# Kernel optimization log

Measured on AMD Instinct MI355X. Metric: run time of the kernel, lower is better.

## Reference

```python
import jax, jax.numpy as jnp
import numpy as np

EPS = 1e-6


def _mlp(x, W1, b1, W2, b2):
    # x: [b,s]; W1: [m,s,h]; W2: [m,h,o] -> [m,b,o]  (m = stacked module dim)
    h = jnp.tanh(jnp.einsum('bs,msh->mbh', x, W1) + b1[:, None, :])
    return jnp.einsum('mbh,mho->mbo', h, W2) + b2[:, None, :]


def _ln(x, g, b):
    mu = jnp.mean(x, axis=-1, keepdims=True)
    var = jnp.var(x, axis=-1, keepdims=True)
    return g * (x - mu) / jnp.sqrt(var + EPS) + b


def setup_inputs() -> dict:
    B, S, H, E, R, L = 1024, 256, 512, 64, 32, 9
    key = jax.random.key(0)
    ks = jax.random.split(key, 8)

    def xavier(k, shape):
        bound = np.sqrt(6.0 / (shape[-2] + shape[-1])).astype(np.float32)
        return jax.random.uniform(k, shape, jnp.float32, -bound, bound)

    return {
        'query_embed': jax.random.normal(ks[0], (B, S), jnp.float32),
        'tpr': jax.random.normal(ks[1], (B, E, R, E), jnp.float32) * 0.1,
        'eW1': xavier(ks[2], (2, S, H)), 'eb1': jnp.zeros((2, H), jnp.float32),
        'eW2': xavier(ks[3], (2, H, E)), 'eb2': jnp.zeros((2, E), jnp.float32),
        'rW1': xavier(ks[4], (3, S, H)), 'rb1': jnp.zeros((3, H), jnp.float32),
        'rW2': xavier(ks[5], (3, H, R)), 'rb2': jnp.zeros((3, R), jnp.float32),
        'ln_g': jnp.ones((3, E), jnp.float32), 'ln_b': jnp.zeros((3, E), jnp.float32),
        'Z': xavier(ks[6], (E, L)),
    }


def reference(query_embed, tpr, eW1, eb1, eW2, eb2, rW1, rb1, rW2, rb2, ln_g, ln_b, Z):
    e = _mlp(query_embed, eW1, eb1, eW2, eb2)   # [2,B,E] (e[1] unused, as in original)
    r = _mlp(query_embed, rW1, rb1, rW2, rb2)   # [3,B,R]
    i1 = _ln(jnp.einsum('be,br,berf->bf', e[0], r[0], tpr), ln_g[0], ln_b[0])
    i2 = _ln(jnp.einsum('be,br,berf->bf', i1, r[1], tpr), ln_g[1], ln_b[1])
    i3 = _ln(jnp.einsum('be,br,berf->bf', i2, r[2], tpr), ln_g[2], ln_b[2])
    step_sum = i1 + i2 + i3
    return jnp.einsum('bf,fl->bl', step_sum, Z)
```

## Files before the change

### kernel.cpp

```cpp
#include <hip/hip_runtime.h>
#include <math.h>

#define B_  1024
#define S_  256
#define H_  512
#define E_  64
#define R_  32
#define L_  9
#define EPS_ 1e-6f
#define TB  16

__global__ __launch_bounds__(256) void mlp_kernel(
    const float* __restrict__ x,
    const float* __restrict__ eW1, const float* __restrict__ eb1,
    const float* __restrict__ eW2, const float* __restrict__ eb2,
    const float* __restrict__ rW1, const float* __restrict__ rb1,
    const float* __restrict__ rW2, const float* __restrict__ rb2,
    float* __restrict__ e0_out,
    float* __restrict__ r_out)
{
    __shared__ float xs[TB][S_];
    __shared__ float hs[TB][H_];
    const int t  = threadIdx.x;
    const int b0 = blockIdx.x * TB;
    const int m  = blockIdx.y;

    #pragma unroll
    for (int i = 0; i < TB; ++i)
        xs[i][t] = x[(size_t)(b0 + i) * S_ + t];
    __syncthreads();

    const float* W1 = (m == 0) ? eW1 : (rW1 + (size_t)(m - 1) * S_ * H_);
    const float* b1 = (m == 0) ? eb1 : (rb1 + (size_t)(m - 1) * H_);

    float acc0[TB], acc1[TB];
    #pragma unroll
    for (int bb = 0; bb < TB; ++bb) { acc0[bb] = 0.0f; acc1[bb] = 0.0f; }

    for (int s = 0; s < S_; ++s) {
        float w0 = W1[(size_t)s * H_ + t];
        float w1 = W1[(size_t)s * H_ + t + 256];
        #pragma unroll
        for (int bb = 0; bb < TB; ++bb) {
            float xv = xs[bb][s];
            acc0[bb] = fmaf(xv, w0, acc0[bb]);
            acc1[bb] = fmaf(xv, w1, acc1[bb]);
        }
    }
    float bias0 = b1[t], bias1 = b1[t + 256];
    #pragma unroll
    for (int bb = 0; bb < TB; ++bb) {
        hs[bb][t]       = tanhf(acc0[bb] + bias0);
        hs[bb][t + 256] = tanhf(acc1[bb] + bias1);
    }
    __syncthreads();

    if (m == 0) {
        const float* W2 = eW2;
        const float* b2 = eb2;
        int o  = t & 63;
        int bq = t >> 6;
        #pragma unroll
        for (int i = 0; i < TB / 4; ++i) {
            int bb = bq + i * 4;
            float acc = b2[o];
            for (int j = 0; j < H_; ++j)
                acc = fmaf(hs[bb][j], W2[(size_t)j * E_ + o], acc);
            e0_out[(size_t)(b0 + bb) * E_ + o] = acc;
        }
    } else {
        const float* W2 = rW2 + (size_t)(m - 1) * H_ * R_;
        const float* b2 = rb2 + (size_t)(m - 1) * R_;
        int o  = t & 31;
        int bq = t >> 5;
        #pragma unroll
        for (int i = 0; i < TB / 8; ++i) {
            int bb = bq + i * 8;
            float acc = b2[o];
            for (int j = 0; j < H_; ++j)
                acc = fmaf(hs[bb][j], W2[(size_t)j * R_ + o], acc);
            r_out[((size_t)(m - 1) * B_ + (b0 + bb)) * R_ + o] = acc;
        }
    }
}

__global__ __launch_bounds__(256) void tpr_kernel(
    const float* __restrict__ tpr,
    const float* __restrict__ e0,
    const float* __restrict__ rws,
    const float* __restrict__ ln_g,
    const float* __restrict__ ln_b,
    const float* __restrict__ Z,
    float* __restrict__ out)
{
    __shared__ __align__(16) float M[3][E_][E_];
    __shared__ float xcur[E_];
    __shared__ float ssum_sh[E_];
    __shared__ float rsh[3][R_];

    const int t = threadIdx.x;
    const int b = blockIdx.x;

    if (t < 96) { int k = t >> 5, j = t & 31; rsh[k][j] = rws[((size_t)k * B_ + b) * R_ + j]; }
    if (t < E_) xcur[t] = e0[(size_t)b * E_ + t];
    __syncthreads();

    const float4* tpr4 = (const float4*)(tpr + (size_t)b * E_ * R_ * E_);
    const int f4 = t & 15;
    const int eg = t >> 4;

    #pragma unroll
    for (int ep = 0; ep < 4; ++ep) {
        int e = eg + 16 * ep;
        float4 a0 = {0, 0, 0, 0}, a1 = {0, 0, 0, 0}, a2 = {0, 0, 0, 0};
        for (int r = 0; r < R_; ++r) {
            float4 v = tpr4[e * 512 + r * 16 + f4];
            float w0 = rsh[0][r], w1 = rsh[1][r], w2 = rsh[2][r];
            a0.x = fmaf(w0, v.x, a0.x); a0.y = fmaf(w0, v.y, a0.y);
            a0.z = fmaf(w0, v.z, a0.z); a0.w = fmaf(w0, v.w, a0.w);
            a1.x = fmaf(w1, v.x, a1.x); a1.y = fmaf(w1, v.y, a1.y);
            a1.z = fmaf(w1, v.z, a1.z); a1.w = fmaf(w1, v.w, a1.w);
            a2.x = fmaf(w2, v.x, a2.x); a2.y = fmaf(w2, v.y, a2.y);
            a2.z = fmaf(w2, v.z, a2.z); a2.w = fmaf(w2, v.w, a2.w);
        }
        ((float4*)&M[0][e][0])[f4] = a0;
        ((float4*)&M[1][e][0])[f4] = a1;
        ((float4*)&M[2][e][0])[f4] = a2;
    }
    __syncthreads();

    float ssum = 0.0f;
    for (int k = 0; k < 3; ++k) {
        float iv = 0.0f;
        if (t < E_) {
            const int f = t;
            float acc = 0.0f;
            for (int e = 0; e < E_; ++e)
                acc = fmaf(xcur[e], M[k][e][f], acc);
            float s = acc;
            #pragma unroll
            for (int off = 32; off >= 1; off >>= 1) s += __shfl_xor(s, off, 64);
            float mu = s * (1.0f / 64.0f);
            float d = acc - mu;
            float vs = d * d;
            #pragma unroll
            for (int off = 32; off >= 1; off >>= 1) vs += __shfl_xor(vs, off, 64);
            float var = vs * (1.0f / 64.0f);
            iv = ln_g[k * E_ + f] * d * rsqrtf(var + EPS_) + ln_b[k * E_ + f];
            ssum += iv;
        }
        __syncthreads();
        if (t < E_) xcur[t] = iv;
        __syncthreads();
    }

    if (t < E_) ssum_sh[t] = ssum;
    __syncthreads();

    if (t < L_) {
        float acc = 0.0f;
        for (int f = 0; f < E_; ++f)
            acc = fmaf(ssum_sh[f], Z[f * L_ + t], acc);
        out[(size_t)b * L_ + t] = acc;
    }
}

extern "C" void kernel_launch(void* const* d_in, const int* in_sizes, int n_in,
                              void* d_out, int out_size, void* d_ws, size_t ws_size,
                              hipStream_t stream) {
    const float* x    = (const float*)d_in[0];
    const float* tpr  = (const float*)d_in[1];
    const float* eW1  = (const float*)d_in[2];
    const float* eb1  = (const float*)d_in[3];
    const float* eW2  = (const float*)d_in[4];
    const float* eb2  = (const float*)d_in[5];
    const float* rW1  = (const float*)d_in[6];
    const float* rb1  = (const float*)d_in[7];
    const float* rW2  = (const float*)d_in[8];
    const float* rb2  = (const float*)d_in[9];
    const float* ln_g = (const float*)d_in[10];
    const float* ln_b = (const float*)d_in[11];
    const float* Z    = (const float*)d_in[12];
    float* out = (float*)d_out;

    float* e0_ws = (float*)d_ws;
    float* r_ws  = e0_ws + (size_t)B_ * E_;

    dim3 g1(B_ / TB, 4);
    mlp_kernel<<<g1, 256, 0, stream>>>(x, eW1, eb1, eW2, eb2,
                                       rW1, rb1, rW2, rb2, e0_ws, r_ws);
    tpr_kernel<<<B_, 256, 0, stream>>>(tpr, e0_ws, r_ws, ln_g, ln_b, Z, out);
}
```

Measured before the change: 793.3 us.

## Split TPR contraction into separate wide build kernel and chain kernel

Moves construction of the three per-batch 64x64 matrices into its own kernel launched over four times as many blocks, writing them to workspace. A second kernel loads these matrices into shared memory and runs the layernorm chain and final projection. This aims to raise parallelism and memory-level parallelism on the large tpr stream. In exchange it adds a global write and read-back of the intermediate matrices and an extra launch. It also adds some unroll pragmas.

```diff
diff --git a/kernel.cpp b/kernel.cpp
--- a/kernel.cpp
+++ b/kernel.cpp
@@ -84,10 +84,46 @@
     }
 }
 
-__global__ __launch_bounds__(256) void tpr_kernel(
+__global__ __launch_bounds__(256) void build_m_kernel(
     const float* __restrict__ tpr,
+    const float* __restrict__ rws,
+    float* __restrict__ Mws)
+{
+    __shared__ float rsh[3][R_];
+    const int t = threadIdx.x;
+    const int b = blockIdx.x;
+    const int ey = blockIdx.y;
+
+    if (t < 96) { int k = t >> 5, j = t & 31; rsh[k][j] = rws[((size_t)k * B_ + b) * R_ + j]; }
+    __syncthreads();
+
+    const int f4 = t & 15;
+    const int e  = (t >> 4) + 16 * ey;
+
+    const float4* row = (const float4*)(tpr + (size_t)b * E_ * R_ * E_) + (size_t)e * 512;
+
+    float4 a0 = {0, 0, 0, 0}, a1 = {0, 0, 0, 0}, a2 = {0, 0, 0, 0};
+    #pragma unroll 8
+    for (int r = 0; r < R_; ++r) {
+        float4 v = row[r * 16 + f4];
+        float w0 = rsh[0][r], w1 = rsh[1][r], w2 = rsh[2][r];
+        a0.x = fmaf(w0, v.x, a0.x); a0.y = fmaf(w0, v.y, a0.y);
+        a0.z = fmaf(w0, v.z, a0.z); a0.w = fmaf(w0, v.w, a0.w);
+        a1.x = fmaf(w1, v.x, a1.x); a1.y = fmaf(w1, v.y, a1.y);
+        a1.z = fmaf(w1, v.z, a1.z); a1.w = fmaf(w1, v.w, a1.w);
+        a2.x = fmaf(w2, v.x, a2.x); a2.y = fmaf(w2, v.y, a2.y);
+        a2.z = fmaf(w2, v.z, a2.z); a2.w = fmaf(w2, v.w, a2.w);
+    }
+
+    float4* M4 = (float4*)(Mws + (size_t)b * 3 * E_ * E_);
+    M4[(0 * E_ + e) * 16 + f4] = a0;
+    M4[(1 * E_ + e) * 16 + f4] = a1;
+    M4[(2 * E_ + e) * 16 + f4] = a2;
+}
+
+__global__ __launch_bounds__(256) void chain_kernel(
+    const float* __restrict__ Mws,
     const float* __restrict__ e0,
-    const float* __restrict__ rws,
     const float* __restrict__ ln_g,
     const float* __restrict__ ln_b,
     const float* __restrict__ Z,
@@ -96,37 +132,17 @@
     __shared__ __align__(16) float M[3][E_][E_];
     __shared__ float xcur[E_];
     __shared__ float ssum_sh[E_];
-    __shared__ float rsh[3][R_];
 
     const int t = threadIdx.x;
     const int b = blockIdx.x;
 
-    if (t < 96) { int k = t >> 5, j = t & 31; rsh[k][j] = rws[((size_t)k * B_ + b) * R_ + j]; }
+    const float4* src = (const float4*)(Mws + (size_t)b * 3 * E_ * E_);
+    float4* dst = (float4*)&M[0][0][0];
+    #pragma unroll
+    for (int i = 0; i < 12; ++i)
+        dst[t + 256 * i] = src[t + 256 * i];
+
     if (t < E_) xcur[t] = e0[(size_t)b * E_ + t];
-    __syncthreads();
-
-    const float4* tpr4 = (const float4*)(tpr + (size_t)b * E_ * R_ * E_);
-    const int f4 = t & 15;
-    const int eg = t >> 4;
-
-    #pragma unroll
-    for (int ep = 0; ep < 4; ++ep) {
-        int e = eg + 16 * ep;
-        float4 a0 = {0, 0, 0, 0}, a1 = {0, 0, 0, 0}, a2 = {0, 0, 0, 0};
-        for (int r = 0; r < R_; ++r) {
-            float4 v = tpr4[e * 512 + r * 16 + f4];
-            float w0 = rsh[0][r], w1 = rsh[1][r], w2 = rsh[2][r];
-            a0.x = fmaf(w0, v.x, a0.x); a0.y = fmaf(w0, v.y, a0.y);
-            a0.z = fmaf(w0, v.z, a0.z); a0.w = fmaf(w0, v.w, a0.w);
-            a1.x = fmaf(w1, v.x, a1.x); a1.y = fmaf(w1, v.y, a1.y);
-            a1.z = fmaf(w1, v.z, a1.z); a1.w = fmaf(w1, v.w, a1.w);
-            a2.x = fmaf(w2, v.x, a2.x); a2.y = fmaf(w2, v.y, a2.y);
-            a2.z = fmaf(w2, v.z, a2.z); a2.w = fmaf(w2, v.w, a2.w);
-        }
-        ((float4*)&M[0][e][0])[f4] = a0;
-        ((float4*)&M[1][e][0])[f4] = a1;
-        ((float4*)&M[2][e][0])[f4] = a2;
-    }
     __syncthreads();
 
     float ssum = 0.0f;
@@ -135,6 +151,7 @@
         if (t < E_) {
             const int f = t;
             float acc = 0.0f;
+            #pragma unroll 8
             for (int e = 0; e < E_; ++e)
                 acc = fmaf(xcur[e], M[k][e][f], acc);
             float s = acc;
@@ -159,6 +176,7 @@
 
     if (t < L_) {
         float acc = 0.0f;
+        #pragma unroll
         for (int f = 0; f < E_; ++f)
             acc = fmaf(ssum_sh[f], Z[f * L_ + t], acc);
         out[(size_t)b * L_ + t] = acc;
@@ -185,9 +203,12 @@
 
     float* e0_ws = (float*)d_ws;
     float* r_ws  = e0_ws + (size_t)B_ * E_;
+    float* M_ws  = r_ws + (size_t)3 * B_ * R_;
 
     dim3 g1(B_ / TB, 4);
     mlp_kernel<<<g1, 256, 0, stream>>>(x, eW1, eb1, eW2, eb2,
                                        rW1, rb1, rW2, rb2, e0_ws, r_ws);
-    tpr_kernel<<<B_, 256, 0, stream>>>(tpr, e0_ws, r_ws, ln_g, ln_b, Z, out);
-}
+    dim3 g2(B_, 4);
+    build_m_kernel<<<g2, 256, 0, stream>>>(tpr, r_ws, M_ws);
+    chain_kernel<<<B_, 256, 0, stream>>>(M_ws, e0_ws, ln_g, ln_b, Z, out);
+}
```

Result: slower. 817.8 us (+3.1%).

## Fold first TPR step into M build and run LN chain in one wavefront

Applied to the files above, without the earlier changes.

The MLP kernel's batch tile is halved so the grid has twice as many blocks, and the R-projection stage is simplified to one row per thread. In the TPR kernel, the first step's contraction with e0 happens while the M matrices are built. Partial sums go into a small shared reduction buffer, so only two M slices are stored. The three layernorm steps and the Z projection then run inside the first 64-thread wavefront with no block-wide barriers. This relies on wavefront-synchronous shared-memory writes and reads of xcur and ssum_sh within a 64-wide wave, and that reliance is fragile.

```diff
diff --git a/kernel.cpp b/kernel.cpp
--- a/kernel.cpp
+++ b/kernel.cpp
@@ -8,7 +8,7 @@
 #define R_  32
 #define L_  9
 #define EPS_ 1e-6f
-#define TB  16
+#define TB  8
 
 __global__ __launch_bounds__(256) void mlp_kernel(
     const float* __restrict__ x,
@@ -72,15 +72,11 @@
         const float* W2 = rW2 + (size_t)(m - 1) * H_ * R_;
         const float* b2 = rb2 + (size_t)(m - 1) * R_;
         int o  = t & 31;
-        int bq = t >> 5;
-        #pragma unroll
-        for (int i = 0; i < TB / 8; ++i) {
-            int bb = bq + i * 8;
-            float acc = b2[o];
-            for (int j = 0; j < H_; ++j)
-                acc = fmaf(hs[bb][j], W2[(size_t)j * R_ + o], acc);
-            r_out[((size_t)(m - 1) * B_ + (b0 + bb)) * R_ + o] = acc;
-        }
+        int bb = t >> 5;
+        float acc = b2[o];
+        for (int j = 0; j < H_; ++j)
+            acc = fmaf(hs[bb][j], W2[(size_t)j * R_ + o], acc);
+        r_out[((size_t)(m - 1) * B_ + (b0 + bb)) * R_ + o] = acc;
     }
 }
 
@@ -93,26 +89,30 @@
     const float* __restrict__ Z,
     float* __restrict__ out)
 {
-    __shared__ __align__(16) float M[3][E_][E_];
+    __shared__ __align__(16) float M[2][E_][E_];
+    __shared__ __align__(16) float red[16][E_];
     __shared__ float xcur[E_];
     __shared__ float ssum_sh[E_];
     __shared__ float rsh[3][R_];
+    __shared__ float e0sh[E_];
 
     const int t = threadIdx.x;
     const int b = blockIdx.x;
 
     if (t < 96) { int k = t >> 5, j = t & 31; rsh[k][j] = rws[((size_t)k * B_ + b) * R_ + j]; }
-    if (t < E_) xcur[t] = e0[(size_t)b * E_ + t];
+    if (t < E_) e0sh[t] = e0[(size_t)b * E_ + t];
     __syncthreads();
 
     const float4* tpr4 = (const float4*)(tpr + (size_t)b * E_ * R_ * E_);
     const int f4 = t & 15;
     const int eg = t >> 4;
 
+    float4 t0p = {0, 0, 0, 0};
     #pragma unroll
     for (int ep = 0; ep < 4; ++ep) {
         int e = eg + 16 * ep;
         float4 a0 = {0, 0, 0, 0}, a1 = {0, 0, 0, 0}, a2 = {0, 0, 0, 0};
+        #pragma unroll 8
         for (int r = 0; r < R_; ++r) {
             float4 v = tpr4[e * 512 + r * 16 + f4];
             float w0 = rsh[0][r], w1 = rsh[1][r], w2 = rsh[2][r];
@@ -123,20 +123,24 @@
             a2.x = fmaf(w2, v.x, a2.x); a2.y = fmaf(w2, v.y, a2.y);
             a2.z = fmaf(w2, v.z, a2.z); a2.w = fmaf(w2, v.w, a2.w);
         }
-        ((float4*)&M[0][e][0])[f4] = a0;
-        ((float4*)&M[1][e][0])[f4] = a1;
-        ((float4*)&M[2][e][0])[f4] = a2;
-    }
-    __syncthreads();
-
-    float ssum = 0.0f;
-    for (int k = 0; k < 3; ++k) {
-        float iv = 0.0f;
-        if (t < E_) {
-            const int f = t;
-            float acc = 0.0f;
-            for (int e = 0; e < E_; ++e)
-                acc = fmaf(xcur[e], M[k][e][f], acc);
+        ((float4*)&M[0][e][0])[f4] = a1;
+        ((float4*)&M[1][e][0])[f4] = a2;
+        float ev = e0sh[e];
+        t0p.x = fmaf(ev, a0.x, t0p.x); t0p.y = fmaf(ev, a0.y, t0p.y);
+        t0p.z = fmaf(ev, a0.z, t0p.z); t0p.w = fmaf(ev, a0.w, t0p.w);
+    }
+    ((float4*)&red[eg][0])[f4] = t0p;
+    __syncthreads();
+
+    if (t < E_) {
+        const int f = t;
+        float acc = 0.0f;
+        #pragma unroll
+        for (int g = 0; g < 16; ++g) acc += red[g][f];
+
+        float ssum = 0.0f;
+        #pragma unroll
+        for (int k = 0; k < 3; ++k) {
             float s = acc;
             #pragma unroll
             for (int off = 32; off >= 1; off >>= 1) s += __shfl_xor(s, off, 64);
@@ -146,22 +150,26 @@
             #pragma unroll
             for (int off = 32; off >= 1; off >>= 1) vs += __shfl_xor(vs, off, 64);
             float var = vs * (1.0f / 64.0f);
-            iv = ln_g[k * E_ + f] * d * rsqrtf(var + EPS_) + ln_b[k * E_ + f];
+            float iv = ln_g[k * E_ + f] * d * rsqrtf(var + EPS_) + ln_b[k * E_ + f];
             ssum += iv;
-        }
-        __syncthreads();
-        if (t < E_) xcur[t] = iv;
-        __syncthreads();
-    }
-
-    if (t < E_) ssum_sh[t] = ssum;
-    __syncthreads();
-
-    if (t < L_) {
-        float acc = 0.0f;
-        for (int f = 0; f < E_; ++f)
-            acc = fmaf(ssum_sh[f], Z[f * L_ + t], acc);
-        out[(size_t)b * L_ + t] = acc;
+            if (k < 2) {
+                xcur[f] = iv;
+                float na = 0.0f;
+                #pragma unroll 8
+                for (int e = 0; e < E_; ++e)
+                    na = fmaf(xcur[e], M[k][e][f], na);
+                acc = na;
+            }
+        }
+        ssum_sh[f] = ssum;
+
+        if (t < L_) {
+            float o = 0.0f;
+            #pragma unroll
+            for (int f2 = 0; f2 < E_; ++f2)
+                o = fmaf(ssum_sh[f2], Z[f2 * L_ + t], o);
+            out[(size_t)b * L_ + t] = o;
+        }
     }
 }
 
```

Result: faster. 756.5 us (-4.6%).
